# Kernel tuning notes

Measured on AMD Instinct MI355X. Metric: run time of the kernel, lower is better.

## Reference

```python
import jax, jax.numpy as jnp
import numpy as np

IN_DIM = 28 * 28   # 784, hard-coded in the torch module
HIDDEN = 1024
OUT_DIM = 10
BATCH = 256
P_KEEP = 0.5       # torch.bernoulli(p * ones) -> keep probability p


def setup_inputs() -> dict:
    key = jax.random.key(0)
    ks = jax.random.split(key, 8)
    x = jax.random.normal(ks[0], (BATCH, IN_DIM), dtype=jnp.float32)
    # Bernoulli(p) mask over (out, in, batch), as in drop_connect
    mask = (jax.random.uniform(ks[1], (HIDDEN, IN_DIM, BATCH)) < P_KEEP).astype(jnp.float32)
    # xavier_uniform with relu gain = sqrt(2)
    def xavier(k, fan_out, fan_in):
        gain = np.sqrt(2.0)
        bound = gain * np.sqrt(6.0 / (fan_in + fan_out))
        return jax.random.uniform(k, (fan_out, fan_in), minval=-bound, maxval=bound, dtype=jnp.float32)
    W1 = xavier(ks[2], HIDDEN, IN_DIM)
    b1 = jnp.zeros((HIDDEN,), jnp.float32)
    W2 = xavier(ks[3], HIDDEN, HIDDEN)
    b2 = jnp.zeros((HIDDEN,), jnp.float32)
    W3 = xavier(ks[4], OUT_DIM, HIDDEN)
    b3 = jnp.zeros((OUT_DIM,), jnp.float32)
    return {"x": x, "mask": mask, "W1": W1, "b1": b1, "W2": W2, "b2": b2, "W3": W3, "b3": b3}


def reference(x, mask, W1, b1, W2, b2, W3, b3):
    # DropConnect layer 1: per-sample masked weight.
    # torch loop: result[b] = (W1 * mask[:, :, b]) @ x[b] + b1
    h1 = jnp.einsum('hi,hib,bi->bh', W1, mask, x) + b1   # [B, H]
    h1 = jax.nn.relu(h1)
    h2 = jax.nn.relu(h1 @ W2.T + b2)                      # [B, H]
    out = h2 @ W3.T + b3                                  # [B, 10]
    return out
```

## Files before the change

### kernel.cpp

```cpp
#include <hip/hip_runtime.h>
#include <hip/hip_bf16.h>

#define IN_DIM 784
#define HIDDEN 1024
#define OUT_DIM 10
#define BATCH 256

#define C_I 49
#define N_CH 16
#define H_T 32

typedef float __attribute__((ext_vector_type(4))) f32x4;

__global__ __launch_bounds__(256) void k_transpose_x(
    const float* __restrict__ x, float* __restrict__ xT)
{
    const int i = blockIdx.x;
    const int b = threadIdx.x;
    xT[i * BATCH + b] = x[b * IN_DIM + i];
}

__global__ __launch_bounds__(1024, 8) void k_layer1_split(
    const float* __restrict__ W1, const float* __restrict__ mask,
    const float* __restrict__ xT, float* __restrict__ partial)
{
    const int ht   = blockIdx.x;
    const int c    = blockIdx.y;
    const int h0   = ht * H_T;
    const int i0   = c * C_I;
    const int t    = threadIdx.x;
    const int bg   = t & 63;
    const int slot = t >> 6;

    __shared__ f32x4 xs[C_I][64];
    __shared__ float wsh[H_T][C_I];

    {
        const f32x4* src = (const f32x4*)(xT + i0 * BATCH);
        f32x4* dst = &xs[0][0];
        for (int idx = t; idx < C_I * 64; idx += 1024)
            dst[idx] = src[idx];
    }
    {
        float* dst = &wsh[0][0];
        for (int idx = t; idx < H_T * C_I; idx += 1024) {
            const int hh = idx / C_I, ii = idx - hh * C_I;
            dst[idx] = W1[(h0 + hh) * IN_DIM + i0 + ii];
        }
    }
    __syncthreads();

    f32x4 acc[2];
    #pragma unroll
    for (int k = 0; k < 2; k++) {
        const int hh = slot * 2 + k;
        const int h  = h0 + hh;
        const f32x4* mrow =
            (const f32x4*)(mask + ((size_t)h * IN_DIM + i0) * BATCH) + bg;
        f32x4 a = {0.f, 0.f, 0.f, 0.f};
        #pragma unroll 2
        for (int i = 0; i < C_I; i++) {
            const f32x4 m  = __builtin_nontemporal_load(mrow + i * 64);
            const f32x4 xv = xs[i][bg];
            const float w  = wsh[hh][i];
            a.x = fmaf(w, m.x * xv.x, a.x);
            a.y = fmaf(w, m.y * xv.y, a.y);
            a.z = fmaf(w, m.z * xv.z, a.z);
            a.w = fmaf(w, m.w * xv.w, a.w);
        }
        acc[k] = a;
    }

    #pragma unroll
    for (int k = 0; k < 2; k++) {
        const int h = h0 + slot * 2 + k;
        __builtin_nontemporal_store(
            acc[k], (f32x4*)partial + ((size_t)c * HIDDEN + h) * 64 + bg);
    }
}

__global__ __launch_bounds__(256) void k_reduce_h1(
    const float* __restrict__ partial, const float* __restrict__ b1,
    float* __restrict__ h1T)
{
    const int t  = threadIdx.x;
    const int bg = t & 63;
    const int h  = blockIdx.x * 4 + (t >> 6);

    const f32x4* p4 = (const f32x4*)partial;
    f32x4 s = {0.f, 0.f, 0.f, 0.f};
    #pragma unroll
    for (int cc = 0; cc < N_CH; cc++) {
        const f32x4 v = __builtin_nontemporal_load(
            p4 + ((size_t)cc * HIDDEN + h) * 64 + bg);
        s.x += v.x; s.y += v.y; s.z += v.z; s.w += v.w;
    }
    const float b = b1[h];
    f32x4 r;
    r.x = fmaxf(s.x + b, 0.f);
    r.y = fmaxf(s.y + b, 0.f);
    r.z = fmaxf(s.z + b, 0.f);
    r.w = fmaxf(s.w + b, 0.f);
    ((f32x4*)h1T)[h * 64 + bg] = r;
}

__global__ __launch_bounds__(256) void k_layer2(
    const float* __restrict__ h1T, const float* __restrict__ W2,
    const float* __restrict__ b2, float* __restrict__ h2)
{
    const int t  = threadIdx.x;
    const int jj = t & 31;
    const int bg = t >> 5;
    const int b0 = blockIdx.x * 32;
    const int j0 = blockIdx.y * 32;

    __shared__ __align__(16) float Ash[32][32];
    __shared__ float Bsh[32][33];

    float acc0 = 0.f, acc1 = 0.f, acc2 = 0.f, acc3 = 0.f;

    for (int h0 = 0; h0 < HIDDEN; h0 += 32) {
        #pragma unroll
        for (int r = 0; r < 4; r++) {
            const int idx = t + r * 256;
            const int hh = idx >> 5, bb = idx & 31;
            Ash[hh][bb] = h1T[(h0 + hh) * BATCH + b0 + bb];
        }
        #pragma unroll
        for (int r = 0; r < 4; r++) {
            const int idx = t + r * 256;
            const int jl = idx >> 5, hl = idx & 31;
            Bsh[hl][jl] = W2[(j0 + jl) * HIDDEN + h0 + hl];
        }
        __syncthreads();
        #pragma unroll 8
        for (int hh = 0; hh < 32; hh++) {
            const float w = Bsh[hh][jj];
            const float4 a = *(const float4*)&Ash[hh][bg * 4];
            acc0 = fmaf(a.x, w, acc0);
            acc1 = fmaf(a.y, w, acc1);
            acc2 = fmaf(a.z, w, acc2);
            acc3 = fmaf(a.w, w, acc3);
        }
        __syncthreads();
    }

    const float bias = b2[j0 + jj];
    const int base = (b0 + bg * 4) * HIDDEN + j0 + jj;
    h2[base + 0 * HIDDEN] = fmaxf(acc0 + bias, 0.f);
    h2[base + 1 * HIDDEN] = fmaxf(acc1 + bias, 0.f);
    h2[base + 2 * HIDDEN] = fmaxf(acc2 + bias, 0.f);
    h2[base + 3 * HIDDEN] = fmaxf(acc3 + bias, 0.f);
}

__global__ __launch_bounds__(256) void k_layer3(
    const float* __restrict__ h2, const float* __restrict__ W3,
    const float* __restrict__ b3, float* __restrict__ out)
{
    const int b = blockIdx.x;
    const int t = threadIdx.x;
    const int lane = t & 63, wid = t >> 6;

    __shared__ float hbuf[HIDDEN];
    #pragma unroll
    for (int r = 0; r < 4; r++)
        hbuf[t + r * 256] = h2[b * HIDDEN + t + r * 256];
    __syncthreads();

    float acc[OUT_DIM];
    #pragma unroll
    for (int o = 0; o < OUT_DIM; o++) acc[o] = 0.f;

    for (int h = t; h < HIDDEN; h += 256) {
        const float v = hbuf[h];
        #pragma unroll
        for (int o = 0; o < OUT_DIM; o++)
            acc[o] = fmaf(v, W3[o * HIDDEN + h], acc[o]);
    }

    __shared__ float red[4][OUT_DIM];
    #pragma unroll
    for (int o = 0; o < OUT_DIM; o++) {
        float v = acc[o];
        for (int off = 32; off > 0; off >>= 1)
            v += __shfl_down(v, off);
        if (lane == 0) red[wid][o] = v;
    }
    __syncthreads();
    if (t < OUT_DIM) {
        out[b * OUT_DIM + t] =
            red[0][t] + red[1][t] + red[2][t] + red[3][t] + b3[t];
    }
}

extern "C" void kernel_launch(void* const* d_in, const int* in_sizes, int n_in,
                              void* d_out, int out_size, void* d_ws, size_t ws_size,
                              hipStream_t stream) {
    const float* x    = (const float*)d_in[0];
    const float* mask = (const float*)d_in[1];
    const float* W1   = (const float*)d_in[2];
    const float* b1   = (const float*)d_in[3];
    const float* W2   = (const float*)d_in[4];
    const float* b2   = (const float*)d_in[5];
    const float* W3   = (const float*)d_in[6];
    const float* b3   = (const float*)d_in[7];
    float* out = (float*)d_out;

    float* ws      = (float*)d_ws;
    float* xT      = ws;
    float* h1T     = xT + IN_DIM * BATCH;
    float* h2      = h1T + HIDDEN * BATCH;
    float* partial = h2 + BATCH * HIDDEN;

    k_transpose_x<<<IN_DIM, 256, 0, stream>>>(x, xT);
    k_layer1_split<<<dim3(HIDDEN / H_T, N_CH), 1024, 0, stream>>>(W1, mask, xT, partial);
    k_reduce_h1<<<HIDDEN / 4, 256, 0, stream>>>(partial, b1, h1T);
    k_layer2<<<dim3(BATCH / 32, HIDDEN / 32), 256, 0, stream>>>(h1T, W2, b2, h2);
    k_layer3<<<BATCH, 256, 0, stream>>>(h2, W3, b3, out);
}
```

Baseline: 1.051 ms.

## Interleave two mask streams, use cached partial stores, double-buffer layer2 tiles

Layer 1 now processes both hidden rows in one loop, issuing two independent nontemporal mask loads per iteration. This raises memory-level parallelism on the dominant mask stream. The partial-sum stores and the loads in the reduction now use normal cached accesses, so the reduction may hit in cache. Layer 2 gains register-staged double buffering in shared memory, prefetching the next tile's global loads while computing the current one, at the cost of extra shared memory and registers.

```diff
diff --git a/kernel.cpp b/kernel.cpp
--- a/kernel.cpp
+++ b/kernel.cpp
@@ -50,33 +50,33 @@
     }
     __syncthreads();
 
-    f32x4 acc[2];
-    #pragma unroll
-    for (int k = 0; k < 2; k++) {
-        const int hh = slot * 2 + k;
-        const int h  = h0 + hh;
-        const f32x4* mrow =
-            (const f32x4*)(mask + ((size_t)h * IN_DIM + i0) * BATCH) + bg;
-        f32x4 a = {0.f, 0.f, 0.f, 0.f};
-        #pragma unroll 2
-        for (int i = 0; i < C_I; i++) {
-            const f32x4 m  = __builtin_nontemporal_load(mrow + i * 64);
-            const f32x4 xv = xs[i][bg];
-            const float w  = wsh[hh][i];
-            a.x = fmaf(w, m.x * xv.x, a.x);
-            a.y = fmaf(w, m.y * xv.y, a.y);
-            a.z = fmaf(w, m.z * xv.z, a.z);
-            a.w = fmaf(w, m.w * xv.w, a.w);
-        }
-        acc[k] = a;
-    }
-
-    #pragma unroll
-    for (int k = 0; k < 2; k++) {
-        const int h = h0 + slot * 2 + k;
-        __builtin_nontemporal_store(
-            acc[k], (f32x4*)partial + ((size_t)c * HIDDEN + h) * 64 + bg);
-    }
+    const int hh0 = slot * 2;
+    const f32x4* mrow0 =
+        (const f32x4*)(mask + ((size_t)(h0 + hh0) * IN_DIM + i0) * BATCH) + bg;
+    const f32x4* mrow1 = mrow0 + (size_t)IN_DIM * 64;
+
+    f32x4 a0 = {0.f, 0.f, 0.f, 0.f};
+    f32x4 a1 = {0.f, 0.f, 0.f, 0.f};
+    #pragma unroll 2
+    for (int i = 0; i < C_I; i++) {
+        const f32x4 m0 = __builtin_nontemporal_load(mrow0 + i * 64);
+        const f32x4 m1 = __builtin_nontemporal_load(mrow1 + i * 64);
+        const f32x4 xv = xs[i][bg];
+        const float w0 = wsh[hh0][i];
+        const float w1 = wsh[hh0 + 1][i];
+        a0.x = fmaf(w0, m0.x * xv.x, a0.x);
+        a0.y = fmaf(w0, m0.y * xv.y, a0.y);
+        a0.z = fmaf(w0, m0.z * xv.z, a0.z);
+        a0.w = fmaf(w0, m0.w * xv.w, a0.w);
+        a1.x = fmaf(w1, m1.x * xv.x, a1.x);
+        a1.y = fmaf(w1, m1.y * xv.y, a1.y);
+        a1.z = fmaf(w1, m1.z * xv.z, a1.z);
+        a1.w = fmaf(w1, m1.w * xv.w, a1.w);
+    }
+
+    f32x4* p4 = (f32x4*)partial + ((size_t)c * HIDDEN + h0 + hh0) * 64 + bg;
+    p4[0]  = a0;
+    p4[64] = a1;
 }
 
 __global__ __launch_bounds__(256) void k_reduce_h1(
@@ -91,8 +91,7 @@
     f32x4 s = {0.f, 0.f, 0.f, 0.f};
     #pragma unroll
     for (int cc = 0; cc < N_CH; cc++) {
-        const f32x4 v = __builtin_nontemporal_load(
-            p4 + ((size_t)cc * HIDDEN + h) * 64 + bg);
+        const f32x4 v = p4[((size_t)cc * HIDDEN + h) * 64 + bg];
         s.x += v.x; s.y += v.y; s.z += v.z; s.w += v.w;
     }
     const float b = b1[h];
@@ -114,35 +113,62 @@
     const int b0 = blockIdx.x * 32;
     const int j0 = blockIdx.y * 32;
 
-    __shared__ __align__(16) float Ash[32][32];
-    __shared__ float Bsh[32][33];
+    __shared__ __align__(16) float Ash[2][32][32];
+    __shared__ float Bsh[2][32][33];
+
+    int a_hh[4], a_bb[4], b_jl[4], b_hl[4];
+    #pragma unroll
+    for (int r = 0; r < 4; r++) {
+        const int idx = t + r * 256;
+        a_hh[r] = idx >> 5; a_bb[r] = idx & 31;
+        b_jl[r] = idx >> 5; b_hl[r] = idx & 31;
+    }
+
+    float ra[4], rb[4];
+    #pragma unroll
+    for (int r = 0; r < 4; r++) {
+        ra[r] = h1T[a_hh[r] * BATCH + b0 + a_bb[r]];
+        rb[r] = W2[(j0 + b_jl[r]) * HIDDEN + b_hl[r]];
+    }
+    #pragma unroll
+    for (int r = 0; r < 4; r++) {
+        Ash[0][a_hh[r]][a_bb[r]] = ra[r];
+        Bsh[0][b_hl[r]][b_jl[r]] = rb[r];
+    }
+    __syncthreads();
 
     float acc0 = 0.f, acc1 = 0.f, acc2 = 0.f, acc3 = 0.f;
 
-    for (int h0 = 0; h0 < HIDDEN; h0 += 32) {
-        #pragma unroll
-        for (int r = 0; r < 4; r++) {
-            const int idx = t + r * 256;
-            const int hh = idx >> 5, bb = idx & 31;
-            Ash[hh][bb] = h1T[(h0 + hh) * BATCH + b0 + bb];
-        }
-        #pragma unroll
-        for (int r = 0; r < 4; r++) {
-            const int idx = t + r * 256;
-            const int jl = idx >> 5, hl = idx & 31;
-            Bsh[hl][jl] = W2[(j0 + jl) * HIDDEN + h0 + hl];
-        }
-        __syncthreads();
+    const int NK = HIDDEN / 32;
+    for (int k = 0; k < NK; k++) {
+        const int cur = k & 1;
+        if (k + 1 < NK) {
+            const int h0n = (k + 1) * 32;
+            #pragma unroll
+            for (int r = 0; r < 4; r++) {
+                ra[r] = h1T[(h0n + a_hh[r]) * BATCH + b0 + a_bb[r]];
+                rb[r] = W2[(j0 + b_jl[r]) * HIDDEN + h0n + b_hl[r]];
+            }
+        }
         #pragma unroll 8
         for (int hh = 0; hh < 32; hh++) {
-            const float w = Bsh[hh][jj];
-            const float4 a = *(const float4*)&Ash[hh][bg * 4];
+            const float w = Bsh[cur][hh][jj];
+            const float4 a = *(const float4*)&Ash[cur][hh][bg * 4];
             acc0 = fmaf(a.x, w, acc0);
             acc1 = fmaf(a.y, w, acc1);
             acc2 = fmaf(a.z, w, acc2);
             acc3 = fmaf(a.w, w, acc3);
         }
         __syncthreads();
+        if (k + 1 < NK) {
+            const int nxt = cur ^ 1;
+            #pragma unroll
+            for (int r = 0; r < 4; r++) {
+                Ash[nxt][a_hh[r]][a_bb[r]] = ra[r];
+                Bsh[nxt][b_hl[r]][b_jl[r]] = rb[r];
+            }
+            __syncthreads();
+        }
     }
 
     const float bias = b2[j0 + jj];
```

Result: no change. 1.047 ms (-0.5%).
